# Kernel optimization log

Measured on AMD Instinct MI355X. Metric: run time of the kernel, lower is better.

Reference implementation:

```python
import jax, jax.numpy as jnp
import numpy as np

N_ATOMS = 20000
N_CG = 1000
N_EDGES = 200000
FEAT = 128
N_RBF = 20
N_CONV = 3
CUTOFF = 5.0
EPS = 1e-15


def swish(x):
    return x * jax.nn.sigmoid(x)


def preprocess_r(r):
    # r: (n, 3) -> dist (n,), unit (n, 3)
    d = jnp.sqrt((r * r + EPS).sum(-1))
    return d, r / d[:, None]


def dist_embed(d, W, b):
    # PainnRadialBasis (learnable_k=False) + Dense + cosine envelope
    k = jnp.arange(1, N_RBF + 1, dtype=d.dtype)
    rbf = jnp.sin(k[None, :] * jnp.pi * d[:, None] / CUTOFF) / d[:, None]
    env = 0.5 * (jnp.cos(jnp.pi * d / CUTOFF) + 1.0) * (d < CUTOFF).astype(d.dtype)
    return (rbf @ W + b) * env[:, None]


def scatter_mean(x, idx, n):
    s = jax.ops.segment_sum(x, idx, num_segments=n)
    cnt = jax.ops.segment_sum(jnp.ones(idx.shape[0], x.dtype), idx, num_segments=n)
    cnt = jnp.maximum(cnt, 1.0)
    return s / cnt.reshape((n,) + (1,) * (x.ndim - 1))


def cg_encoder(z, xyz, cg_xyz, mapping, nbr_list, embed,
               msg_W1, msg_b1, msg_W2, msg_b2, msg_distW, msg_distb,
               upd_U, upd_V, upd_W1, upd_b1, upd_W2, upd_b2,
               cg_W1, cg_b1, cg_W2, cg_b2, cg_distW, cg_distb):
    s = embed[z]                                     # (N, F)
    v = jnp.zeros((s.shape[0], FEAT, 3), s.dtype)    # (N, F, 3)
    src, dst = nbr_list[:, 0], nbr_list[:, 1]
    r_ij = xyz[dst] - xyz[src]
    r_iI = xyz - cg_xyz[mapping]
    d_ij, u_ij = preprocess_r(r_ij)
    d_iI, u_iI = preprocess_r(r_iI)

    S_I = None
    V_I = None
    for i in range(N_CONV):
        # ---- MessageBlock ----
        phi = swish(s @ msg_W1[i] + msg_b1[i]) @ msg_W2[i] + msg_b2[i]          # (N, 3F)
        w_s = dist_embed(d_ij, msg_distW[i], msg_distb[i])                      # (E, 3F)
        inv = (phi[dst] * w_s).reshape(-1, 3, FEAT)                             # (E, 3, F)
        dv_ij = inv[:, 2, :, None] * u_ij[:, None, :] + inv[:, 0, :, None] * v[dst]
        s = s + jax.ops.segment_sum(inv[:, 1, :], src, num_segments=N_ATOMS)
        v = v + jax.ops.segment_sum(dv_ij, src, num_segments=N_ATOMS)
        # ---- UpdateBlock ----
        u_v = jnp.einsum('nfd,fg->ngd', v, upd_U[i])
        v_v = jnp.einsum('nfd,fg->ngd', v, upd_V[i])
        v_v_norm = jnp.sqrt((v_v * v_v + EPS).sum(-1))                          # (N, F)
        stack = swish(jnp.concatenate([s, v_v_norm], -1) @ upd_W1[i] + upd_b1[i]) @ upd_W2[i] + upd_b2[i]
        a_vv = stack[:, :FEAT, None]
        a_sv = stack[:, FEAT:2 * FEAT]
        a_ss = stack[:, 2 * FEAT:]
        v = v + u_v * a_vv
        s = s + (u_v * v_v).sum(-1) * a_sv + a_ss
        # ---- init CG features after first conv ----
        if i == 0:
            S_I = scatter_mean(s, mapping, N_CG)
            V_I = jnp.zeros((N_CG, FEAT, 3), s.dtype)
        # ---- ContractiveMessageBlock ----
        phi_cg = swish(s @ cg_W1[i] + cg_b1[i]) @ cg_W2[i] + cg_b2[i]           # (N, 3F)
        w_cg = dist_embed(d_iI, cg_distW[i], cg_distb[i])
        inv_cg = (phi_cg * w_cg).reshape(-1, 3, FEAT)
        dv_iI = inv_cg[:, 2, :, None] * u_iI[:, None, :] + inv_cg[:, 0, :, None] * v
        S_I = S_I + scatter_mean(inv_cg[:, 1, :], mapping, N_CG)
        V_I = V_I + scatter_mean(dv_iI, mapping, N_CG)
    return S_I


def setup_inputs() -> dict:
    key = jax.random.key(0)
    ks = jax.random.split(key, 20)
    p = lambda i, shape: jax.random.normal(ks[i], shape, jnp.float32) * 0.05
    return {
        'z': jax.random.randint(ks[0], (N_ATOMS,), 1, 100),
        'xyz': jax.random.normal(ks[1], (N_ATOMS, 3), jnp.float32),
        'cg_xyz': jax.random.normal(ks[2], (N_CG, 3), jnp.float32),
        'mapping': jax.random.randint(ks[3], (N_ATOMS,), 0, N_CG),
        'nbr_list': jax.random.randint(ks[4], (N_EDGES, 2), 0, N_ATOMS),
        'embed': p(5, (100, FEAT)).at[0].set(0.0),  # padding_idx=0
        'msg_W1': p(6, (N_CONV, FEAT, FEAT)), 'msg_b1': jnp.zeros((N_CONV, FEAT)),
        'msg_W2': p(7, (N_CONV, FEAT, 3 * FEAT)), 'msg_b2': jnp.zeros((N_CONV, 3 * FEAT)),
        'msg_distW': p(8, (N_CONV, N_RBF, 3 * FEAT)), 'msg_distb': jnp.zeros((N_CONV, 3 * FEAT)),
        'upd_U': p(9, (N_CONV, FEAT, FEAT)), 'upd_V': p(10, (N_CONV, FEAT, FEAT)),
        'upd_W1': p(11, (N_CONV, 2 * FEAT, FEAT)), 'upd_b1': jnp.zeros((N_CONV, FEAT)),
        'upd_W2': p(12, (N_CONV, FEAT, 3 * FEAT)), 'upd_b2': jnp.zeros((N_CONV, 3 * FEAT)),
        'cg_W1': p(13, (N_CONV, FEAT, FEAT)), 'cg_b1': jnp.zeros((N_CONV, FEAT)),
        'cg_W2': p(14, (N_CONV, FEAT, 3 * FEAT)), 'cg_b2': jnp.zeros((N_CONV, 3 * FEAT)),
        'cg_distW': p(15, (N_CONV, N_RBF, 3 * FEAT)), 'cg_distb': jnp.zeros((N_CONV, 3 * FEAT)),
    }


def reference(z, xyz, cg_xyz, mapping, nbr_list, embed,
              msg_W1, msg_b1, msg_W2, msg_b2, msg_distW, msg_distb,
              upd_U, upd_V, upd_W1, upd_b1, upd_W2, upd_b2,
              cg_W1, cg_b1, cg_W2, cg_b2, cg_distW, cg_distb):
    return cg_encoder(z, xyz, cg_xyz, mapping, nbr_list, embed,
                      msg_W1, msg_b1, msg_W2, msg_b2, msg_distW, msg_distb,
                      upd_U, upd_V, upd_W1, upd_b1, upd_W2, upd_b2,
                      cg_W1, cg_b1, cg_W2, cg_b2, cg_distW, cg_distb)
```

## Files before the change

kernel.cpp:

```cpp
#include <hip/hip_runtime.h>
#include <math.h>

#define N_ATOMS 20000
#define N_CG    1000
#define N_EDGES 200000
#define FEAT    128
#define NRBF    20
#define NCONV   3
#define CUTOFF  5.0f
#define PLANE   (N_ATOMS * FEAT)
#define PI_F    3.14159265358979323846f
#define LDH     130
#define SPAD    136

#define PACK_PER_CONV 212992

typedef __attribute__((ext_vector_type(8))) short bf16x8;
typedef __attribute__((ext_vector_type(4))) float f32x4;

__device__ __forceinline__ void split2(float x, ushort& h, ushort& l)
{
    unsigned u  = __float_as_uint(x);
    unsigned hb = (u + 0x7FFFu + ((u >> 16) & 1u)) & 0xFFFF0000u;
    float    hf = __uint_as_float(hb);
    float    lf = x - hf;
    unsigned ul = __float_as_uint(lf);
    h = (ushort)(hb >> 16);
    l = (ushort)((ul + 0x7FFFu + ((ul >> 16) & 1u)) >> 16);
}

__device__ __forceinline__ float reconP(unsigned u)
{
    return __uint_as_float(u & 0xFFFF0000u) + __uint_as_float(u << 16);
}

__device__ __forceinline__ unsigned packP(float x)
{
    ushort h, l;
    split2(x, h, l);
    return ((unsigned)h << 16) | l;
}

__device__ __forceinline__ void splitv8(const float* hv, bf16x8& ah, bf16x8& al)
{
#pragma unroll
    for (int j = 0; j < 8; ++j) {
        ushort h, l;
        split2(hv[j], h, l);
        ah[j] = (short)h; al[j] = (short)l;
    }
}

__device__ __forceinline__ void unpack8(const unsigned* __restrict__ p,
                                        bf16x8& ah, bf16x8& al)
{
#pragma unroll
    for (int j = 0; j < 8; ++j) {
        unsigned u = p[j];
        ah[j] = (short)(u >> 16);
        al[j] = (short)(u & 0xFFFFu);
    }
}

#define MFMA3(ACC, AH_, AL_, BH_, BL_)                                              \
    ACC = __builtin_amdgcn_mfma_f32_16x16x32_bf16(AH_, BH_, ACC, 0, 0, 0);          \
    ACC = __builtin_amdgcn_mfma_f32_16x16x32_bf16(AH_, BL_, ACC, 0, 0, 0);          \
    ACC = __builtin_amdgcn_mfma_f32_16x16x32_bf16(AL_, BH_, ACC, 0, 0, 0);

template<int K1, int N2>
__global__ __launch_bounds__(256)
void mlp_fused(const ushort* __restrict__ AH, const ushort* __restrict__ AL,
               const ushort* __restrict__ B1h, const ushort* __restrict__ B1l,
               const float* __restrict__ b1,
               const ushort* __restrict__ B2h, const ushort* __restrict__ B2l,
               const float* __restrict__ b2, int bcol0,
               float* __restrict__ C)
{
    __shared__ float Hs[32 * LDH];
    const int tid  = threadIdx.x;
    const int lane = tid & 63;
    const int w    = tid >> 6;
    const int wm   = w & 1, wn = w >> 1;
    const int m0   = blockIdx.x * 32;
    const int l15  = lane & 15;
    const int koff = (lane >> 4) * 8;
    const int rowb = wm * 16;
    const int q4   = (lane >> 4) * 4;

    f32x4 acc1[4];
#pragma unroll
    for (int j = 0; j < 4; ++j) acc1[j] = (f32x4){0.f, 0.f, 0.f, 0.f};
#pragma unroll
    for (int k0 = 0; k0 < K1; k0 += 32) {
        size_t aa = (size_t)(m0 + rowb + l15) * K1 + k0 + koff;
        bf16x8 ah = *reinterpret_cast<const bf16x8*>(AH + aa);
        bf16x8 al = *reinterpret_cast<const bf16x8*>(AL + aa);
#pragma unroll
        for (int nf = 0; nf < 4; ++nf) {
            size_t ba = (size_t)(wn * 64 + nf * 16 + l15) * K1 + k0 + koff;
            bf16x8 bh = *reinterpret_cast<const bf16x8*>(B1h + ba);
            bf16x8 bl = *reinterpret_cast<const bf16x8*>(B1l + ba);
            MFMA3(acc1[nf], ah, al, bh, bl);
        }
    }
#pragma unroll
    for (int nf = 0; nf < 4; ++nf) {
        int col = wn * 64 + nf * 16 + l15;
        float bv = b1[col];
#pragma unroll
        for (int r = 0; r < 4; ++r) {
            float x = acc1[nf][r] + bv;
            x = x / (1.f + __expf(-x));
            Hs[(rowb + q4 + r) * LDH + col] = x;
        }
    }
    __syncthreads();

    constexpr int NF2  = N2 / 32;
    constexpr int WCOL = N2 / 2;
    f32x4 acc2[NF2];
#pragma unroll
    for (int j = 0; j < NF2; ++j) acc2[j] = (f32x4){0.f, 0.f, 0.f, 0.f};
#pragma unroll
    for (int k0 = 0; k0 < 128; k0 += 32) {
        const float* hp = &Hs[(rowb + l15) * LDH + k0 + koff];
        float hv[8];
#pragma unroll
        for (int j = 0; j < 8; ++j) hv[j] = hp[j];
        bf16x8 ah, al;
        splitv8(hv, ah, al);
#pragma unroll
        for (int nf = 0; nf < NF2; ++nf) {
            size_t ba = (size_t)(wn * WCOL + nf * 16 + l15) * 128 + k0 + koff;
            bf16x8 bh = *reinterpret_cast<const bf16x8*>(B2h + ba);
            bf16x8 bl = *reinterpret_cast<const bf16x8*>(B2l + ba);
            MFMA3(acc2[nf], ah, al, bh, bl);
        }
    }
#pragma unroll
    for (int nf = 0; nf < NF2; ++nf) {
        int col = wn * WCOL + nf * 16 + l15;
        float bv = b2 ? b2[bcol0 + col] : 0.f;
#pragma unroll
        for (int r = 0; r < 4; ++r) {
            int row = m0 + rowb + q4 + r;
            C[(size_t)row * N2 + col] = acc2[nf][r] + bv;
        }
    }
}

template<int HAS_MSG>
__global__ __launch_bounds__(512, 4)
void k_update_mega(unsigned* __restrict__ vP,
                   const ushort* __restrict__ catH, const ushort* __restrict__ catL,
                   const ushort* __restrict__ BVh, const ushort* __restrict__ BVl,
                   const ushort* __restrict__ W1h, const ushort* __restrict__ W1l,
                   const float*  __restrict__ b1,
                   const ushort* __restrict__ W2h, const ushort* __restrict__ W2l,
                   const float*  __restrict__ b2,
                   const ushort* __restrict__ BUh, const ushort* __restrict__ BUl,
                   float* __restrict__ s,
                   const ushort* __restrict__ M1h, const ushort* __restrict__ M1l,
                   const float*  __restrict__ m1b,
                   const ushort* __restrict__ M2h, const ushort* __restrict__ M2l,
                   const float*  __restrict__ m2b,
                   const ushort* __restrict__ C1h, const ushort* __restrict__ C1l,
                   const float*  __restrict__ c1b,
                   const ushort* __restrict__ C2h, const ushort* __restrict__ C2l,
                   const float*  __restrict__ c2b,
                   float* __restrict__ phi, float* __restrict__ uv)
{
    __shared__ __align__(16) char smem[16640 + 17408 + 16640];
    float*  Hs  = (float*)smem;
    ushort* nH  = (ushort*)(smem + 16640);
    ushort* nL  = (ushort*)(smem + 16640 + 32 * SPAD * 2);
    ushort* sHs = nH;
    ushort* sLs = nL;
    float*  Hc  = (float*)(smem + 16640 + 17408);

    const int tid  = threadIdx.x;
    const int lane = tid & 63;
    const int w    = tid >> 6;
    const int wm   = w & 1, wn = w >> 1;
    const int m0   = blockIdx.x * 32;
    const int l15  = lane & 15;
    const int koff = (lane >> 4) * 8;
    const int rowb = wm * 16;
    const int q4   = (lane >> 4) * 4;

    f32x4 accV[3][2], accU[3][2];
#pragma unroll
    for (int d = 0; d < 3; ++d)
#pragma unroll
        for (int j = 0; j < 2; ++j) {
            accV[d][j] = (f32x4){0.f, 0.f, 0.f, 0.f};
            accU[d][j] = (f32x4){0.f, 0.f, 0.f, 0.f};
        }
#pragma unroll
    for (int k0 = 0; k0 < 128; k0 += 32) {
        bf16x8 ah[3], al[3];
#pragma unroll
        for (int d = 0; d < 3; ++d) {
            size_t aa = (size_t)d * PLANE + (size_t)(m0 + rowb + l15) * 128 + k0 + koff;
            unsigned u[8];
#pragma unroll
            for (int j = 0; j < 8; ++j) u[j] = vP[aa + j];
            unpack8(u, ah[d], al[d]);
        }
#pragma unroll
        for (int nf = 0; nf < 2; ++nf) {
            size_t ba = (size_t)(wn * 32 + nf * 16 + l15) * 128 + k0 + koff;
            bf16x8 bvh = *reinterpret_cast<const bf16x8*>(BVh + ba);
            bf16x8 bvl = *reinterpret_cast<const bf16x8*>(BVl + ba);
            bf16x8 buh = *reinterpret_cast<const bf16x8*>(BUh + ba);
            bf16x8 bul = *reinterpret_cast<const bf16x8*>(BUl + ba);
#pragma unroll
            for (int d = 0; d < 3; ++d) {
                MFMA3(accV[d][nf], ah[d], al[d], bvh, bvl);
            }
#pragma unroll
            for (int d = 0; d < 3; ++d) {
                MFMA3(accU[d][nf], ah[d], al[d], buh, bul);
            }
        }
    }
#pragma unroll
    for (int nf = 0; nf < 2; ++nf) {
        int col = wn * 32 + nf * 16 + l15;
#pragma unroll
        for (int r = 0; r < 4; ++r) {
            int lrow = rowb + q4 + r;
            float x = accV[0][nf][r], y = accV[1][nf][r], z = accV[2][nf][r];
            float nrm = sqrtf(x * x + y * y + z * z + 3e-15f);
            ushort h, l;
            split2(nrm, h, l);
            nH[lrow * SPAD + col] = h;
            nL[lrow * SPAD + col] = l;
        }
    }
    __syncthreads();

    f32x4 acc1[2];
#pragma unroll
    for (int j = 0; j < 2; ++j) acc1[j] = (f32x4){0.f, 0.f, 0.f, 0.f};
#pragma unroll
    for (int k0 = 0; k0 < 256; k0 += 32) {
        bf16x8 ah, al;
        if (k0 < 128) {
            size_t aa = (size_t)(m0 + rowb + l15) * 128 + k0 + koff;
            ah = *reinterpret_cast<const bf16x8*>(catH + aa);
            al = *reinterpret_cast<const bf16x8*>(catL + aa);
        } else {
            int la = (rowb + l15) * SPAD + (k0 - 128) + koff;
            ah = *reinterpret_cast<const bf16x8*>(nH + la);
            al = *reinterpret_cast<const bf16x8*>(nL + la);
        }
#pragma unroll
        for (int nf = 0; nf < 2; ++nf) {
            size_t ba = (size_t)(wn * 32 + nf * 16 + l15) * 256 + k0 + koff;
            bf16x8 bh = *reinterpret_cast<const bf16x8*>(W1h + ba);
            bf16x8 bl = *reinterpret_cast<const bf16x8*>(W1l + ba);
            MFMA3(acc1[nf], ah, al, bh, bl);
        }
    }
#pragma unroll
    for (int nf = 0; nf < 2; ++nf) {
        int col = wn * 32 + nf * 16 + l15;
        float bv = b1[col];
#pragma unroll
        for (int r = 0; r < 4; ++r) {
            float x = acc1[nf][r] + bv;
            x = x / (1.f + __expf(-x));
            Hs[(rowb + q4 + r) * LDH + col] = x;
        }
    }
    __syncthreads();

    f32x4 acc2[6];
#pragma unroll
    for (int j = 0; j < 6; ++j) acc2[j] = (f32x4){0.f, 0.f, 0.f, 0.f};
#pragma unroll
    for (int k0 = 0; k0 < 128; k0 += 32) {
        const float* hp = &Hs[(rowb + l15) * LDH + k0 + koff];
        float hv[8];
#pragma unroll
        for (int j = 0; j < 8; ++j) hv[j] = hp[j];
        bf16x8 ah, al;
        splitv8(hv, ah, al);
#pragma unroll
        for (int g = 0; g < 3; ++g) {
#pragma unroll
            for (int j = 0; j < 2; ++j) {
                size_t ba = (size_t)(g * 128 + wn * 32 + j * 16 + l15) * 128 + k0 + koff;
                bf16x8 bh = *reinterpret_cast<const bf16x8*>(W2h + ba);
                bf16x8 bl = *reinterpret_cast<const bf16x8*>(W2l + ba);
                MFMA3(acc2[g * 2 + j], ah, al, bh, bl);
            }
        }
    }

#pragma unroll
    for (int nf = 0; nf < 2; ++nf) {
        int col = wn * 32 + nf * 16 + l15;
        float bavv = b2[col];
        float basv = b2[128 + col];
        float bass = b2[256 + col];
#pragma unroll
        for (int r = 0; r < 4; ++r) {
            int lrow = rowb + q4 + r;
            int row  = m0 + lrow;
            size_t idx = (size_t)row * FEAT + col;
            float avv = acc2[nf][r]     + bavv;
            float asv = acc2[2 + nf][r] + basv;
            float ass = acc2[4 + nf][r] + bass;
            float u0 = accU[0][nf][r], u1 = accU[1][nf][r], u2 = accU[2][nf][r];
            float w0 = accV[0][nf][r], w1 = accV[1][nf][r], w2 = accV[2][nf][r];
            float dot = u0 * w0 + u1 * w1 + u2 * w2;
            float n0 = reconP(vP[idx])                      + u0 * avv;
            float n1 = reconP(vP[PLANE + idx])              + u1 * avv;
            float n2 = reconP(vP[2 * (size_t)PLANE + idx])  + u2 * avv;
            vP[idx] = packP(n0);
            vP[PLANE + idx] = packP(n1);
            vP[2 * (size_t)PLANE + idx] = packP(n2);
            float ns = s[idx] + dot * asv + ass;
            s[idx] = ns;
            ushort h, l;
            split2(ns, h, l);
            sHs[lrow * SPAD + col] = h;
            sLs[lrow * SPAD + col] = l;
        }
    }
    __syncthreads();

    f32x4 am[2], ac[2];
#pragma unroll
    for (int j = 0; j < 2; ++j) {
        am[j] = (f32x4){0.f, 0.f, 0.f, 0.f};
        ac[j] = (f32x4){0.f, 0.f, 0.f, 0.f};
    }
#pragma unroll
    for (int k0 = 0; k0 < 128; k0 += 32) {
        int la = (rowb + l15) * SPAD + k0 + koff;
        bf16x8 ah = *reinterpret_cast<const bf16x8*>(sHs + la);
        bf16x8 al = *reinterpret_cast<const bf16x8*>(sLs + la);
#pragma unroll
        for (int nf = 0; nf < 2; ++nf) {
            size_t ba = (size_t)(wn * 32 + nf * 16 + l15) * 128 + k0 + koff;
            if (HAS_MSG) {
                bf16x8 bh = *reinterpret_cast<const bf16x8*>(M1h + ba);
                bf16x8 bl = *reinterpret_cast<const bf16x8*>(M1l + ba);
                MFMA3(am[nf], ah, al, bh, bl);
            }
            bf16x8 ch = *reinterpret_cast<const bf16x8*>(C1h + ba);
            bf16x8 cl = *reinterpret_cast<const bf16x8*>(C1l + ba);
            MFMA3(ac[nf], ah, al, ch, cl);
        }
    }
#pragma unroll
    for (int nf = 0; nf < 2; ++nf) {
        int col = wn * 32 + nf * 16 + l15;
        float bvc = c1b[col];
        float bvm = HAS_MSG ? m1b[col] : 0.f;
#pragma unroll
        for (int r = 0; r < 4; ++r) {
            int lr = rowb + q4 + r;
            if (HAS_MSG) {
                float x = am[nf][r] + bvm;
                Hs[lr * LDH + col] = x / (1.f + __expf(-x));
            }
            float y = ac[nf][r] + bvc;
            Hc[lr * LDH + col] = y / (1.f + __expf(-y));
        }
    }
    __syncthreads();

    f32x4 a2m[6], a2c[2];
    if (HAS_MSG) {
#pragma unroll
        for (int j = 0; j < 6; ++j) a2m[j] = (f32x4){0.f, 0.f, 0.f, 0.f};
    }
#pragma unroll
    for (int j = 0; j < 2; ++j)  a2c[j] = (f32x4){0.f, 0.f, 0.f, 0.f};
#pragma unroll
    for (int k0 = 0; k0 < 128; k0 += 32) {
        const float* hpc = &Hc[(rowb + l15) * LDH + k0 + koff];
        float hvc[8];
#pragma unroll
        for (int j = 0; j < 8; ++j) hvc[j] = hpc[j];
        bf16x8 ahc, alc;
        splitv8(hvc, ahc, alc);
#pragma unroll
        for (int nf = 0; nf < 2; ++nf) {
            size_t ba = (size_t)(wn * 32 + nf * 16 + l15) * 128 + k0 + koff;
            bf16x8 bh = *reinterpret_cast<const bf16x8*>(C2h + ba);
            bf16x8 bl = *reinterpret_cast<const bf16x8*>(C2l + ba);
            MFMA3(a2c[nf], ahc, alc, bh, bl);
        }
        if (HAS_MSG) {
            const float* hpm = &Hs[(rowb + l15) * LDH + k0 + koff];
            float hvm[8];
#pragma unroll
            for (int j = 0; j < 8; ++j) hvm[j] = hpm[j];
            bf16x8 ahm, alm;
            splitv8(hvm, ahm, alm);
#pragma unroll
            for (int nf = 0; nf < 6; ++nf) {
                size_t ba = (size_t)(wn * 96 + nf * 16 + l15) * 128 + k0 + koff;
                bf16x8 bh = *reinterpret_cast<const bf16x8*>(M2h + ba);
                bf16x8 bl = *reinterpret_cast<const bf16x8*>(M2l + ba);
                MFMA3(a2m[nf], ahm, alm, bh, bl);
            }
        }
    }
    if (HAS_MSG) {
#pragma unroll
        for (int nf = 0; nf < 6; ++nf) {
            int col = wn * 96 + nf * 16 + l15;
            float bv = m2b[col];
#pragma unroll
            for (int r = 0; r < 4; ++r) {
                int row = m0 + rowb + q4 + r;
                phi[(size_t)row * 384 + col] = a2m[nf][r] + bv;
            }
        }
    }
#pragma unroll
    for (int nf = 0; nf < 2; ++nf) {
        int col = wn * 32 + nf * 16 + l15;
        float bv = c2b[128 + col];
#pragma unroll
        for (int r = 0; r < 4; ++r) {
            int row = m0 + rowb + q4 + r;
            uv[(size_t)row * 128 + col] = a2c[nf][r] + bv;
        }
    }
}

__global__ void k_pack_all(const float* __restrict__ msg_W1, const float* __restrict__ msg_W2,
                           const float* __restrict__ upd_V,  const float* __restrict__ upd_W1,
                           const float* __restrict__ upd_W2, const float* __restrict__ upd_U,
                           const float* __restrict__ cg_W1,  const float* __restrict__ cg_W2,
                           ushort* __restrict__ Bh, ushort* __restrict__ Bl)
{
    const int wid = blockIdx.y, conv = blockIdx.z;
    const float* W; int K, N, ldw, col0; size_t off;
    switch (wid) {
        case 0: W = msg_W1 + (size_t)conv * 16384; K = 128; N = 128; ldw = 128; col0 = 0;   off = 0;      break;
        case 1: W = msg_W2 + (size_t)conv * 49152; K = 128; N = 384; ldw = 384; col0 = 0;   off = 16384;  break;
        case 2: W = upd_V  + (size_t)conv * 16384; K = 128; N = 128; ldw = 128; col0 = 0;   off = 65536;  break;
        case 3: W = upd_W1 + (size_t)conv * 32768; K = 256; N = 128; ldw = 128; col0 = 0;   off = 81920;  break;
        case 4: W = upd_W2 + (size_t)conv * 49152; K = 128; N = 384; ldw = 384; col0 = 0;   off = 114688; break;
        case 5: W = upd_U  + (size_t)conv * 16384; K = 128; N = 128; ldw = 128; col0 = 0;   off = 163840; break;
        case 6: W = cg_W1  + (size_t)conv * 16384; K = 128; N = 128; ldw = 128; col0 = 0;   off = 180224; break;
        default:W = cg_W2  + (size_t)conv * 49152; K = 128; N = 128; ldw = 384; col0 = 128; off = 196608; break;
    }
    off += (size_t)conv * PACK_PER_CONV;
    int idx = blockIdx.x * 256 + threadIdx.x;
    if (idx >= K * N) return;
    int k = idx & (K - 1);
    int n = idx >> ((K == 256) ? 8 : 7);
    ushort h, l;
    split2(W[(size_t)k * ldw + col0 + n], h, l);
    Bh[off + (size_t)n * K + k] = h;
    Bl[off + (size_t)n * K + k] = l;
}

__global__ void k_s_init(const int* __restrict__ z, const float* __restrict__ embed,
                         float* __restrict__ s, ushort* __restrict__ sH, ushort* __restrict__ sL)
{
    int idx = blockIdx.x * blockDim.x + threadIdx.x;
    if (idx >= PLANE) return;
    int n = idx >> 7, g = idx & 127;
    float e = embed[z[n] * FEAT + g];
    s[idx] = e;
    ushort h, l;
    split2(e, h, l);
    sH[idx] = h; sL[idx] = l;
}

__global__ void k_atom_geo(const int* __restrict__ mapping,
                           const float* __restrict__ xyz, const float* __restrict__ cg_xyz,
                           float* __restrict__ rbf_a, float* __restrict__ env_a,
                           float* __restrict__ cnt)
{
    int n = blockIdx.x * blockDim.x + threadIdx.x;
    if (n >= N_ATOMS) return;
    int m = mapping[n];
    float dx = xyz[n * 3 + 0] - cg_xyz[m * 3 + 0];
    float dy = xyz[n * 3 + 1] - cg_xyz[m * 3 + 1];
    float dz = xyz[n * 3 + 2] - cg_xyz[m * 3 + 2];
    float d = sqrtf(dx * dx + dy * dy + dz * dz + 3e-15f);
    float env = (d < CUTOFF) ? 0.5f * (cosf(PI_F * d / CUTOFF) + 1.f) : 0.f;
    env_a[n] = env;
    float s = env / d;
#pragma unroll
    for (int k = 0; k < NRBF; ++k)
        rbf_a[n * NRBF + k] = sinf((k + 1) * PI_F * d / CUTOFF) * s;
    atomicAdd(&cnt[m], 1.f);
}

__global__ void k_deg(const int* __restrict__ nbr, int* __restrict__ deg)
{
    int e = blockIdx.x * blockDim.x + threadIdx.x;
    if (e < N_EDGES) atomicAdd(&deg[nbr[2 * e]], 1);
}

__global__ __launch_bounds__(1024)
void k_scan(const int* __restrict__ deg, int* __restrict__ rowptr)
{
    __shared__ int sh[1024];
    const int chunk = (N_ATOMS + 1023) / 1024;
    int t = threadIdx.x;
    int base = t * chunk;
    int sum = 0;
    for (int i = 0; i < chunk; ++i) {
        int idx = base + i;
        if (idx < N_ATOMS) sum += deg[idx];
    }
    sh[t] = sum;
    __syncthreads();
    for (int off = 1; off < 1024; off <<= 1) {
        int val = (t >= off) ? sh[t - off] : 0;
        __syncthreads();
        sh[t] += val;
        __syncthreads();
    }
    int run = (t == 0) ? 0 : sh[t - 1];
    for (int i = 0; i < chunk; ++i) {
        int idx = base + i;
        if (idx < N_ATOMS) { rowptr[idx] = run; run += deg[idx]; }
    }
}

__global__ void k_fill(const int* __restrict__ nbr, const float* __restrict__ xyz,
                       const int* __restrict__ rowptr, int* __restrict__ cursor,
                       int* __restrict__ rec_dst, float4* __restrict__ rec_u4,
                       float* __restrict__ rec_rbf)
{
    int e = blockIdx.x * blockDim.x + threadIdx.x;
    if (e >= N_EDGES) return;
    int src = nbr[2 * e], dst = nbr[2 * e + 1];
    int pos = atomicAdd(&cursor[src], 1);
    int q = rowptr[src] + pos;
    float dx = xyz[dst * 3 + 0] - xyz[src * 3 + 0];
    float dy = xyz[dst * 3 + 1] - xyz[src * 3 + 1];
    float dz = xyz[dst * 3 + 2] - xyz[src * 3 + 2];
    float d = sqrtf(dx * dx + dy * dy + dz * dz + 3e-15f);
    float env = (d < CUTOFF) ? 0.5f * (cosf(PI_F * d / CUTOFF) + 1.f) : 0.f;
    rec_dst[q] = dst;
    rec_u4[q] = make_float4(dx / d, dy / d, dz / d, env);
    float sc = env / d;
#pragma unroll
    for (int k = 0; k < NRBF; ++k)
        rec_rbf[(size_t)q * NRBF + k] = sinf((k + 1) * PI_F * d / CUTOFF) * sc;
}

#define EDGE_BLOCKS 2500
__global__ __launch_bounds__(512, 2)
void k_edge_seg(const int* __restrict__ rowptr, const int* __restrict__ deg,
                const int* __restrict__ rec_dst, const float4* __restrict__ rec_u4,
                const float* __restrict__ rec_rbf,
                const float* __restrict__ phi,
                const unsigned* __restrict__ vPi, unsigned* __restrict__ vPo,
                float* __restrict__ s,
                ushort* __restrict__ catH, ushort* __restrict__ catL,
                const float* __restrict__ distW, const float* __restrict__ distb)
{
    const int tid    = threadIdx.x;
    const int slot   = tid >> 7;
    const int f      = tid & 127;
    const int slot_g = blockIdx.x * 4 + slot;
    const int nslots = EDGE_BLOCKS * 4;

    float wx[21], wy[21], wz[21];
#pragma unroll
    for (int k = 0; k < NRBF; ++k) {
        wx[k] = distW[k * 384 + f];
        wy[k] = distW[k * 384 + 128 + f];
        wz[k] = distW[k * 384 + 256 + f];
    }
    wx[20] = distb[f];
    wy[20] = distb[128 + f];
    wz[20] = distb[256 + f];
#pragma unroll
    for (int k = 0; k < 21; ++k) {
        asm volatile("" : "+v"(wx[k]), "+v"(wy[k]), "+v"(wz[k]));
    }

    for (int a = slot_g; a < N_ATOMS; a += nslots) {
        const int beg = rowptr[a];
        const int end = beg + deg[a];
        float s_acc = 0.f, vx = 0.f, vy = 0.f, vz = 0.f;

        for (int p = beg; p < end; p += 2) {
            const int  has2 = (p + 1 < end);
            const int  p1   = has2 ? p + 1 : p;
            const float m1  = has2 ? 1.f : 0.f;

            float4 u40 = rec_u4[p];
            float4 u41 = rec_u4[p1];
            int dst0 = rec_dst[p];
            int dst1 = rec_dst[p1];

            const float* ph0 = phi + (size_t)dst0 * 384 + f;
            const float* ph1 = phi + (size_t)dst1 * 384 + f;
            float p00 = ph0[0], p01 = ph0[128], p02 = ph0[256];
            float p10 = ph1[0], p11 = ph1[128], p12 = ph1[256];
            size_t di0 = (size_t)dst0 * FEAT + f;
            size_t di1 = (size_t)dst1 * FEAT + f;
            float v0x = reconP(vPi[di0]);
            float v0y = reconP(vPi[PLANE + di0]);
            float v0z = reconP(vPi[2 * (size_t)PLANE + di0]);
            float v1x = reconP(vPi[di1]);
            float v1y = reconP(vPi[PLANE + di1]);
            float v1z = reconP(vPi[2 * (size_t)PLANE + di1]);
            const float4* rb0 = reinterpret_cast<const float4*>(rec_rbf + (size_t)p  * NRBF);
            const float4* rb1 = reinterpret_cast<const float4*>(rec_rbf + (size_t)p1 * NRBF);
            float4 a0 = rb0[0], a1 = rb0[1], a2 = rb0[2], a3 = rb0[3], a4 = rb0[4];
            float4 b0 = rb1[0], b1 = rb1[1], b2 = rb1[2], b3 = rb1[3], b4 = rb1[4];

            const float rr0[21] = {a0.x, a0.y, a0.z, a0.w, a1.x, a1.y, a1.z, a1.w,
                                   a2.x, a2.y, a2.z, a2.w, a3.x, a3.y, a3.z, a3.w,
                                   a4.x, a4.y, a4.z, a4.w, u40.w};
            const float rr1[21] = {b0.x, b0.y, b0.z, b0.w, b1.x, b1.y, b1.z, b1.w,
                                   b2.x, b2.y, b2.z, b2.w, b3.x, b3.y, b3.z, b3.w,
                                   b4.x, b4.y, b4.z, b4.w, u41.w};
            float w00 = 0.f, w01 = 0.f, w02 = 0.f;
            float w10 = 0.f, w11 = 0.f, w12 = 0.f;
#pragma unroll
            for (int k = 0; k < 21; ++k) {
                w00 += rr0[k] * wx[k];
                w01 += rr0[k] * wy[k];
                w02 += rr0[k] * wz[k];
                w10 += rr1[k] * wx[k];
                w11 += rr1[k] * wy[k];
                w12 += rr1[k] * wz[k];
            }
            float i00 = p00 * w00, i01 = p01 * w01, i02 = p02 * w02;
            float i10 = (p10 * w10) * m1, i11 = (p11 * w11) * m1, i12 = (p12 * w12) * m1;
            vx += i02 * u40.x + i00 * v0x;
            vy += i02 * u40.y + i00 * v0y;
            vz += i02 * u40.z + i00 * v0z;
            s_acc += i01;
            vx += i12 * u41.x + i10 * v1x;
            vy += i12 * u41.y + i10 * v1y;
            vz += i12 * u41.z + i10 * v1z;
            s_acc += i11;
        }

        size_t si = (size_t)a * FEAT + f;
        float ns = s[si] + s_acc;
        s[si] = ns;
        float nx = reconP(vPi[si])                     + vx;
        float ny = reconP(vPi[PLANE + si])             + vy;
        float nz = reconP(vPi[2 * (size_t)PLANE + si]) + vz;
        vPo[si] = packP(nx);
        vPo[PLANE + si] = packP(ny);
        vPo[2 * (size_t)PLANE + si] = packP(nz);
        ushort h, l;
        split2(ns, h, l);
        catH[(size_t)a * 128 + f] = h;
        catL[(size_t)a * 128 + f] = l;
    }
}

__global__ __launch_bounds__(128)
void k_cg_msg(const int* __restrict__ mapping, const float* __restrict__ phi_mid,
              const float* __restrict__ rbf_a, const float* __restrict__ env_a,
              const float* __restrict__ distW, const float* __restrict__ distb,
              const float* __restrict__ s_add, float* __restrict__ S_acc)
{
    int n = blockIdx.x;
    float env = env_a[n];
    int f = threadIdx.x;
    if (env == 0.f && s_add == nullptr) return;
    float val = s_add ? s_add[n * FEAT + f] : 0.f;
    if (env != 0.f) {
        __shared__ float sh_rbf[NRBF];
        if (f < NRBF) sh_rbf[f] = rbf_a[n * NRBF + f];
        __syncthreads();
        float w1 = 0.f;
#pragma unroll
        for (int k = 0; k < NRBF; ++k)
            w1 += sh_rbf[k] * distW[k * 384 + 128 + f];
        w1 += distb[128 + f] * env;
        val += phi_mid[n * FEAT + f] * w1;
    }
    atomicAdd(&S_acc[mapping[n] * FEAT + f], val);
}

__global__ void k_finalize(const float* __restrict__ S_acc, const float* __restrict__ cnt,
                           float* __restrict__ out, int add)
{
    int idx = blockIdx.x * blockDim.x + threadIdx.x;
    if (idx >= N_CG * FEAT) return;
    float val = S_acc[idx] / fmaxf(cnt[idx >> 7], 1.f);
    if (add) out[idx] += val;
    else     out[idx] = val;
}

extern "C" void kernel_launch(void* const* d_in, const int* in_sizes, int n_in,
                              void* d_out, int out_size, void* d_ws, size_t ws_size,
                              hipStream_t stream)
{
    const int*   z        = (const int*)d_in[0];
    const float* xyz      = (const float*)d_in[1];
    const float* cg_xyz   = (const float*)d_in[2];
    const int*   mapping  = (const int*)d_in[3];
    const int*   nbr      = (const int*)d_in[4];
    const float* embed    = (const float*)d_in[5];
    const float* msg_W1   = (const float*)d_in[6];
    const float* msg_b1   = (const float*)d_in[7];
    const float* msg_W2   = (const float*)d_in[8];
    const float* msg_b2   = (const float*)d_in[9];
    const float* msg_dW   = (const float*)d_in[10];
    const float* msg_db   = (const float*)d_in[11];
    const float* upd_U    = (const float*)d_in[12];
    const float* upd_V    = (const float*)d_in[13];
    const float* upd_W1   = (const float*)d_in[14];
    const float* upd_b1   = (const float*)d_in[15];
    const float* upd_W2   = (const float*)d_in[16];
    const float* upd_b2   = (const float*)d_in[17];
    const float* cg_W1    = (const float*)d_in[18];
    const float* cg_b1    = (const float*)d_in[19];
    const float* cg_W2    = (const float*)d_in[20];
    const float* cg_b2    = (const float*)d_in[21];
    const float* cg_dW    = (const float*)d_in[22];
    const float* cg_db    = (const float*)d_in[23];
    float* out = (float*)d_out;

    float* ws = (float*)d_ws;
    size_t o = 0;
    float* s      = ws + o; o += PLANE;
    float* uv     = ws + o; o += PLANE;
    float* phi    = ws + o; o += (size_t)N_ATOMS * 384;
    float* catpk  = ws + o; o += PLANE;
    float* spk    = ws + o; o += PLANE;
    unsigned* vPA = (unsigned*)(ws + o); o += 3 * PLANE;
    unsigned* vPB = (unsigned*)(ws + o); o += 3 * PLANE;
    float4* rec_u4 = (float4*)(ws + o); o += (size_t)N_EDGES * 4;
    float* rec_rbf = ws + o; o += (size_t)N_EDGES * NRBF;
    int*   rec_dst = (int*)(ws + o); o += N_EDGES;
    float* rbf_a  = ws + o; o += (size_t)N_ATOMS * NRBF;
    float* env_a  = ws + o; o += N_ATOMS;
    float* cnt    = ws + o; o += N_CG;
    float* S_acc  = ws + o; o += (size_t)NCONV * N_CG * FEAT;
    int*   deg    = (int*)(ws + o); o += N_ATOMS;
    int*   rowptr = (int*)(ws + o); o += N_ATOMS;
    int*   cursor = (int*)(ws + o); o += N_ATOMS;
    ushort* packH = (ushort*)(ws + o); o += (size_t)NCONV * PACK_PER_CONV / 2;
    ushort* packL = (ushort*)(ws + o); o += (size_t)NCONV * PACK_PER_CONV / 2;

    ushort* catH = (ushort*)catpk; ushort* catL = catH + (size_t)N_ATOMS * 128;
    ushort* sH = (ushort*)spk;  ushort* sL = sH + PLANE;

    hipMemsetAsync(vPA, 0, sizeof(unsigned) * 3 * PLANE, stream);
    hipMemsetAsync(cnt, 0, sizeof(float) * N_CG, stream);
    hipMemsetAsync(deg, 0, sizeof(int) * N_ATOMS, stream);
    hipMemsetAsync(cursor, 0, sizeof(int) * N_ATOMS, stream);
    hipMemsetAsync(S_acc, 0, sizeof(float) * NCONV * N_CG * FEAT, stream);
    k_pack_all<<<dim3(192, 8, 3), 256, 0, stream>>>(msg_W1, msg_W2, upd_V, upd_W1,
                                                    upd_W2, upd_U, cg_W1, cg_W2,
                                                    packH, packL);
    k_s_init<<<(PLANE + 255) / 256, 256, 0, stream>>>(z, embed, s, sH, sL);
    k_atom_geo<<<(N_ATOMS + 255) / 256, 256, 0, stream>>>(mapping, xyz, cg_xyz,
                                                          rbf_a, env_a, cnt);
    k_deg<<<(N_EDGES + 255) / 256, 256, 0, stream>>>(nbr, deg);
    k_scan<<<1, 1024, 0, stream>>>(deg, rowptr);
    k_fill<<<(N_EDGES + 255) / 256, 256, 0, stream>>>(nbr, xyz, rowptr, cursor,
                                                      rec_dst, rec_u4, rec_rbf);

    unsigned* vPc = vPA;
    unsigned* vPn = vPB;

    mlp_fused<128, 384><<<625, 256, 0, stream>>>(
        sH, sL, packH + 0, packL + 0, msg_b1,
        packH + 16384, packL + 16384, msg_b2, 0, phi);

    for (int i = 0; i < NCONV; ++i) {
        const float* ub1 = upd_b1 + (size_t)i * FEAT;
        const float* ub2 = upd_b2 + (size_t)i * 384;
        const float* mdW = msg_dW + (size_t)i * NRBF * 384;
        const float* mdb = msg_db + (size_t)i * 384;
        const float* cb1 = cg_b1  + (size_t)i * FEAT;
        const float* cb2 = cg_b2  + (size_t)i * 384;
        const float* cdW = cg_dW  + (size_t)i * NRBF * 384;
        const float* cdb = cg_db  + (size_t)i * 384;
        const size_t pb  = (size_t)i * PACK_PER_CONV;
        float* Sa = S_acc + (size_t)i * N_CG * FEAT;

        k_edge_seg<<<EDGE_BLOCKS, 512, 0, stream>>>(rowptr, deg, rec_dst, rec_u4,
                                                    rec_rbf, phi, vPc, vPn, s,
                                                    catH, catL, mdW, mdb);

        if (i < NCONV - 1) {
            const size_t pn = (size_t)(i + 1) * PACK_PER_CONV;
            k_update_mega<1><<<625, 512, 0, stream>>>(
                vPn, catH, catL,
                packH + pb + 65536,  packL + pb + 65536,
                packH + pb + 81920,  packL + pb + 81920,
                ub1,
                packH + pb + 114688, packL + pb + 114688,
                ub2,
                packH + pb + 163840, packL + pb + 163840,
                s,
                packH + pn + 0,      packL + pn + 0,
                msg_b1 + (size_t)(i + 1) * FEAT,
                packH + pn + 16384,  packL + pn + 16384,
                msg_b2 + (size_t)(i + 1) * 384,
                packH + pb + 180224, packL + pb + 180224, cb1,
                packH + pb + 196608, packL + pb + 196608, cb2,
                phi, uv);
        } else {
            k_update_mega<0><<<625, 512, 0, stream>>>(
                vPn, catH, catL,
                packH + pb + 65536,  packL + pb + 65536,
                packH + pb + 81920,  packL + pb + 81920,
                ub1,
                packH + pb + 114688, packL + pb + 114688,
                ub2,
                packH + pb + 163840, packL + pb + 163840,
                s,
                nullptr, nullptr, nullptr, nullptr, nullptr, nullptr,
                packH + pb + 180224, packL + pb + 180224, cb1,
                packH + pb + 196608, packL + pb + 196608, cb2,
                phi, uv);
        }

        k_cg_msg<<<N_ATOMS, 128, 0, stream>>>(mapping, uv, rbf_a, env_a, cdW, cdb,
                                              (i == 0) ? s : nullptr, Sa);
        k_finalize<<<(N_CG * FEAT + 255) / 256, 256, 0, stream>>>(Sa, cnt, out,
                                                                  i == 0 ? 0 : 1);

        unsigned* t = vPn; vPn = vPc; vPc = t;
    }
}
```

Before: 1.255 ms.

## Fuse CG message scatter into update kernel and accumulate all convs once

The coarse-grained message computation (radial filter dot product times the uv projection, plus the initial s contribution) moves into the epilogue of the update mega-kernel. Results are atomically added straight into one shared S accumulator, so the uv buffer, the per-atom k_cg_msg launch and the per-conv finalize launches are no longer needed. A single finalize runs at the end. This cuts global traffic and kernel launches, at the cost of more registers in an already heavy kernel, which may lower occupancy.

```diff
diff --git a/kernel.cpp b/kernel.cpp
--- a/kernel.cpp
+++ b/kernel.cpp
@@ -149,7 +149,7 @@
     }
 }
 
-template<int HAS_MSG>
+template<int HAS_MSG, int SADD>
 __global__ __launch_bounds__(512, 4)
 void k_update_mega(unsigned* __restrict__ vP,
                    const ushort* __restrict__ catH, const ushort* __restrict__ catL,
@@ -168,7 +168,11 @@
                    const float*  __restrict__ c1b,
                    const ushort* __restrict__ C2h, const ushort* __restrict__ C2l,
                    const float*  __restrict__ c2b,
-                   float* __restrict__ phi, float* __restrict__ uv)
+                   float* __restrict__ phi,
+                   const float* __restrict__ cdW, const float* __restrict__ cdb,
+                   const int*   __restrict__ mapping,
+                   const float* __restrict__ env_a, const float* __restrict__ rbf_a,
+                   float* __restrict__ S_acc)
 {
     __shared__ __align__(16) char smem[16640 + 17408 + 16640];
     float*  Hs  = (float*)smem;
@@ -299,6 +303,7 @@
         }
     }
 
+    float nsav[2][4];
 #pragma unroll
     for (int nf = 0; nf < 2; ++nf) {
         int col = wn * 32 + nf * 16 + l15;
@@ -324,6 +329,7 @@
             vP[2 * (size_t)PLANE + idx] = packP(n2);
             float ns = s[idx] + dot * asv + ass;
             s[idx] = ns;
+            nsav[nf][r] = ns;
             ushort h, l;
             split2(ns, h, l);
             sHs[lrow * SPAD + col] = h;
@@ -424,14 +430,43 @@
             }
         }
     }
-#pragma unroll
-    for (int nf = 0; nf < 2; ++nf) {
-        int col = wn * 32 + nf * 16 + l15;
-        float bv = c2b[128 + col];
-#pragma unroll
-        for (int r = 0; r < 4; ++r) {
-            int row = m0 + rowb + q4 + r;
-            uv[(size_t)row * 128 + col] = a2c[nf][r] + bv;
+
+    float wc0[21], wc1[21];
+    {
+        int c0 = wn * 32 + l15;
+        int c1 = wn * 32 + 16 + l15;
+#pragma unroll
+        for (int k = 0; k < NRBF; ++k) {
+            wc0[k] = cdW[k * 384 + 128 + c0];
+            wc1[k] = cdW[k * 384 + 128 + c1];
+        }
+        wc0[20] = cdb[128 + c0];
+        wc1[20] = cdb[128 + c1];
+    }
+#pragma unroll
+    for (int r = 0; r < 4; ++r) {
+        int lrow = rowb + q4 + r;
+        int n    = m0 + lrow;
+        float env = env_a[n];
+        int   m   = mapping[n];
+        float rb[NRBF];
+#pragma unroll
+        for (int k = 0; k < NRBF; ++k) rb[k] = rbf_a[(size_t)n * NRBF + k];
+#pragma unroll
+        for (int nf = 0; nf < 2; ++nf) {
+            int col = wn * 32 + nf * 16 + l15;
+            const float* wc = nf ? wc1 : wc0;
+            float val = SADD ? nsav[nf][r] : 0.f;
+            if (env != 0.f) {
+                float w1s = 0.f;
+#pragma unroll
+                for (int k = 0; k < NRBF; ++k) w1s += rb[k] * wc[k];
+                w1s += wc[20] * env;
+                float uvv = a2c[nf][r] + c2b[128 + col];
+                val += uvv * w1s;
+            }
+            if (SADD || env != 0.f)
+                atomicAdd(&S_acc[(size_t)m * FEAT + col], val);
         }
     }
 }
@@ -664,39 +699,12 @@
     }
 }
 
-__global__ __launch_bounds__(128)
-void k_cg_msg(const int* __restrict__ mapping, const float* __restrict__ phi_mid,
-              const float* __restrict__ rbf_a, const float* __restrict__ env_a,
-              const float* __restrict__ distW, const float* __restrict__ distb,
-              const float* __restrict__ s_add, float* __restrict__ S_acc)
-{
-    int n = blockIdx.x;
-    float env = env_a[n];
-    int f = threadIdx.x;
-    if (env == 0.f && s_add == nullptr) return;
-    float val = s_add ? s_add[n * FEAT + f] : 0.f;
-    if (env != 0.f) {
-        __shared__ float sh_rbf[NRBF];
-        if (f < NRBF) sh_rbf[f] = rbf_a[n * NRBF + f];
-        __syncthreads();
-        float w1 = 0.f;
-#pragma unroll
-        for (int k = 0; k < NRBF; ++k)
-            w1 += sh_rbf[k] * distW[k * 384 + 128 + f];
-        w1 += distb[128 + f] * env;
-        val += phi_mid[n * FEAT + f] * w1;
-    }
-    atomicAdd(&S_acc[mapping[n] * FEAT + f], val);
-}
-
 __global__ void k_finalize(const float* __restrict__ S_acc, const float* __restrict__ cnt,
-                           float* __restrict__ out, int add)
+                           float* __restrict__ out)
 {
     int idx = blockIdx.x * blockDim.x + threadIdx.x;
     if (idx >= N_CG * FEAT) return;
-    float val = S_acc[idx] / fmaxf(cnt[idx >> 7], 1.f);
-    if (add) out[idx] += val;
-    else     out[idx] = val;
+    out[idx] = S_acc[idx] / fmaxf(cnt[idx >> 7], 1.f);
 }
 
 extern "C" void kernel_launch(void* const* d_in, const int* in_sizes, int n_in,
@@ -732,7 +740,6 @@
     float* ws = (float*)d_ws;
     size_t o = 0;
     float* s      = ws + o; o += PLANE;
-    float* uv     = ws + o; o += PLANE;
     float* phi    = ws + o; o += (size_t)N_ATOMS * 384;
     float* catpk  = ws + o; o += PLANE;
     float* spk    = ws + o; o += PLANE;
@@ -744,7 +751,7 @@
     float* rbf_a  = ws + o; o += (size_t)N_ATOMS * NRBF;
     float* env_a  = ws + o; o += N_ATOMS;
     float* cnt    = ws + o; o += N_CG;
-    float* S_acc  = ws + o; o += (size_t)NCONV * N_CG * FEAT;
+    float* S_acc  = ws + o; o += N_CG * FEAT;
     int*   deg    = (int*)(ws + o); o += N_ATOMS;
     int*   rowptr = (int*)(ws + o); o += N_ATOMS;
     int*   cursor = (int*)(ws + o); o += N_ATOMS;
@@ -758,7 +765,7 @@
     hipMemsetAsync(cnt, 0, sizeof(float) * N_CG, stream);
     hipMemsetAsync(deg, 0, sizeof(int) * N_ATOMS, stream);
     hipMemsetAsync(cursor, 0, sizeof(int) * N_ATOMS, stream);
-    hipMemsetAsync(S_acc, 0, sizeof(float) * NCONV * N_CG * FEAT, stream);
+    hipMemsetAsync(S_acc, 0, sizeof(float) * N_CG * FEAT, stream);
     k_pack_all<<<dim3(192, 8, 3), 256, 0, stream>>>(msg_W1, msg_W2, upd_V, upd_W1,
                                                     upd_W2, upd_U, cg_W1, cg_W2,
                                                     packH, packL);
@@ -787,51 +794,54 @@
         const float* cdW = cg_dW  + (size_t)i * NRBF * 384;
         const float* cdb = cg_db  + (size_t)i * 384;
         const size_t pb  = (size_t)i * PACK_PER_CONV;
-        float* Sa = S_acc + (size_t)i * N_CG * FEAT;
 
         k_edge_seg<<<EDGE_BLOCKS, 512, 0, stream>>>(rowptr, deg, rec_dst, rec_u4,
                                                     rec_rbf, phi, vPc, vPn, s,
                                                     catH, catL, mdW, mdb);
 
-        if (i < NCONV - 1) {
-            const size_t pn = (size_t)(i + 1) * PACK_PER_CONV;
-            k_update_mega<1><<<625, 512, 0, stream>>>(
+        const size_t pn = (size_t)((i + 1 < NCONV) ? (i + 1) : i) * PACK_PER_CONV;
+        if (i == 0) {
+            k_update_mega<1, 1><<<625, 512, 0, stream>>>(
                 vPn, catH, catL,
                 packH + pb + 65536,  packL + pb + 65536,
-                packH + pb + 81920,  packL + pb + 81920,
-                ub1,
-                packH + pb + 114688, packL + pb + 114688,
-                ub2,
+                packH + pb + 81920,  packL + pb + 81920, ub1,
+                packH + pb + 114688, packL + pb + 114688, ub2,
                 packH + pb + 163840, packL + pb + 163840,
                 s,
-                packH + pn + 0,      packL + pn + 0,
-                msg_b1 + (size_t)(i + 1) * FEAT,
-                packH + pn + 16384,  packL + pn + 16384,
-                msg_b2 + (size_t)(i + 1) * 384,
+                packH + pn + 0,      packL + pn + 0,      msg_b1 + (size_t)(i + 1) * FEAT,
+                packH + pn + 16384,  packL + pn + 16384,  msg_b2 + (size_t)(i + 1) * 384,
                 packH + pb + 180224, packL + pb + 180224, cb1,
                 packH + pb + 196608, packL + pb + 196608, cb2,
-                phi, uv);
-        } else {
-            k_update_mega<0><<<625, 512, 0, stream>>>(
+                phi, cdW, cdb, mapping, env_a, rbf_a, S_acc);
+        } else if (i < NCONV - 1) {
+            k_update_mega<1, 0><<<625, 512, 0, stream>>>(
                 vPn, catH, catL,
                 packH + pb + 65536,  packL + pb + 65536,
-                packH + pb + 81920,  packL + pb + 81920,
-                ub1,
-                packH + pb + 114688, packL + pb + 114688,
-                ub2,
+                packH + pb + 81920,  packL + pb + 81920, ub1,
+                packH + pb + 114688, packL + pb + 114688, ub2,
+                packH + pb + 163840, packL + pb + 163840,
+                s,
+                packH + pn + 0,      packL + pn + 0,      msg_b1 + (size_t)(i + 1) * FEAT,
+                packH + pn + 16384,  packL + pn + 16384,  msg_b2 + (size_t)(i + 1) * 384,
+                packH + pb + 180224, packL + pb + 180224, cb1,
+                packH + pb + 196608, packL + pb + 196608, cb2,
+                phi, cdW, cdb, mapping, env_a, rbf_a, S_acc);
+        } else {
+            k_update_mega<0, 0><<<625, 512, 0, stream>>>(
+                vPn, catH, catL,
+                packH + pb + 65536,  packL + pb + 65536,
+                packH + pb + 81920,  packL + pb + 81920, ub1,
+                packH + pb + 114688, packL + pb + 114688, ub2,
                 packH + pb + 163840, packL + pb + 163840,
                 s,
                 nullptr, nullptr, nullptr, nullptr, nullptr, nullptr,
                 packH + pb + 180224, packL + pb + 180224, cb1,
                 packH + pb + 196608, packL + pb + 196608, cb2,
-                phi, uv);
-        }
-
-        k_cg_msg<<<N_ATOMS, 128, 0, stream>>>(mapping, uv, rbf_a, env_a, cdW, cdb,
-                                              (i == 0) ? s : nullptr, Sa);
-        k_finalize<<<(N_CG * FEAT + 255) / 256, 256, 0, stream>>>(Sa, cnt, out,
-                                                                  i == 0 ? 0 : 1);
+                phi, cdW, cdb, mapping, env_a, rbf_a, S_acc);
+        }
 
         unsigned* t = vPn; vPn = vPc; vPc = t;
     }
-}
+
+    k_finalize<<<(N_CG * FEAT + 255) / 256, 256, 0, stream>>>(S_acc, cnt, out);
+}
```

New measurement: 1.237 ms. About the same (-1.4%).
